# Kernel optimization log

Measured on AMD Instinct MI355X. Metric: run time of the kernel, lower is better.

The kernel has to match this reference:

```python
import jax, jax.numpy as jnp
import numpy as np

B = 8          # batch size (clouds)
NC = 2048      # coarse points per cloud (pos / x)
NF = 8192      # fine points per cloud (pos_skip / x_skip)
C = 256        # coarse feature dim
CS = 64        # skip feature dim
OUT = 256      # MLP output dim
K = 3          # knn_interpolate k (FPParams default)
EPS = 1e-16    # PyG clamp epsilon on squared distance


def setup_inputs() -> dict:
    key = jax.random.key(0)
    ks = jax.random.split(key, 8)
    x = jax.random.normal(ks[0], (B * NC, C), dtype=jnp.float32)
    pos = jax.random.normal(ks[1], (B * NC, 3), dtype=jnp.float32)
    x_skip = jax.random.normal(ks[2], (B * NF, CS), dtype=jnp.float32)
    pos_skip = jax.random.normal(ks[3], (B * NF, 3), dtype=jnp.float32)
    # contiguous, sorted batch assignments (standard PyG layout)
    batch = jnp.repeat(jnp.arange(B, dtype=jnp.int64), NC)
    batch_skip = jnp.repeat(jnp.arange(B, dtype=jnp.int64), NF)
    W1 = jax.random.normal(ks[4], (C + CS, OUT), dtype=jnp.float32) * (1.0 / np.sqrt(C + CS))
    b1 = jnp.zeros((OUT,), dtype=jnp.float32)
    W2 = jax.random.normal(ks[5], (OUT, OUT), dtype=jnp.float32) * (1.0 / np.sqrt(OUT))
    b2 = jnp.zeros((OUT,), dtype=jnp.float32)
    return {"x": x, "pos": pos, "batch": batch, "x_skip": x_skip,
            "pos_skip": pos_skip, "batch_skip": batch_skip,
            "W1": W1, "b1": b1, "W2": W2, "b2": b2}


def _knn_interpolate(x, pos, pos_skip):
    # x: [B*NC, C], pos: [B*NC, 3], pos_skip: [B*NF, 3]
    posb = pos.reshape(B, NC, 3)
    posf = pos_skip.reshape(B, NF, 3)
    xb = x.reshape(B, NC, -1)
    # squared pairwise distances per cloud: [B, NF, NC]
    d2 = jnp.sum((posf[:, :, None, :] - posb[:, None, :, :]) ** 2, axis=-1)
    neg_d2, idx = jax.lax.top_k(-d2, K)          # k nearest -> [B, NF, K]
    d2k = -neg_d2
    w = 1.0 / jnp.maximum(d2k, EPS)              # inverse squared-distance weights
    w = w / jnp.sum(w, axis=-1, keepdims=True)   # [B, NF, K]
    gathered = jax.vmap(lambda xv, iv: xv[iv])(xb, idx)  # [B, NF, K, C]
    out = jnp.sum(gathered * w[..., None], axis=2)       # [B, NF, C]
    return out.reshape(B * NF, -1)


def reference(x, pos, batch, x_skip, pos_skip, batch_skip, W1, b1, W2, b2):
    # 1) interpolate coarse features onto fine points (pos.shape[0] != pos_skip.shape[0])
    xi = _knn_interpolate(x, pos, pos_skip)        # [B*NF, C]
    # 2) concat skip features
    h = jnp.concatenate([xi, x_skip], axis=1)      # [B*NF, C+CS]
    # 3) MLP: Linear -> ReLU -> Linear -> ReLU
    h = jax.nn.relu(h @ W1 + b1)
    h = jax.nn.relu(h @ W2 + b2)
    return (h, pos_skip, batch_skip)
```

## Files before the change

### kernel.cpp

```cpp
#include <hip/hip_runtime.h>
#include <hip/hip_bf16.h>

#define BATCH 8
#define NC 2048
#define NF 8192
#define CDIM 256
#define CSKIP 64
#define OUTD 256
#define MTOT (BATCH*NF)
#define NCTOT (BATCH*NC)
#define NCHUNK 8
#define CHSZ (NC/NCHUNK)

typedef __attribute__((ext_vector_type(8))) short short8;
typedef __attribute__((ext_vector_type(4))) float floatx4;

static __device__ __forceinline__ ushort f2bf(float f) {
    union { float f; unsigned u; } v; v.f = f;
    unsigned r = v.u + 0x7fffu + ((v.u >> 16) & 1u);
    return (ushort)(r >> 16);
}
static __device__ __forceinline__ float bf2f(ushort u) {
    union { unsigned u; float f; } v; v.u = ((unsigned)u) << 16;
    return v.f;
}

#if defined(__has_builtin) && __has_builtin(__builtin_amdgcn_fmed3f)
#define MED3F(a, b, c) __builtin_amdgcn_fmed3f((a), (b), (c))
#else
static __device__ __forceinline__ float MED3F(float a, float b, float c) {
    return fmaxf(fminf(a, b), fminf(fmaxf(a, b), c));
}
#endif

#define TOP3_INS(d, jj, D0, D1, D2, I0, I1, I2)     \
    {                                               \
        bool c2 = (d) < D2, c1 = (d) < D1, c0 = (d) < D0; \
        I2 = c1 ? I1 : (c2 ? (jj) : I2);            \
        I1 = c0 ? I0 : (c1 ? (jj) : I1);            \
        I0 = c0 ? (jj) : I0;                        \
        D2 = MED3F(D1, D2, (d));                    \
        D1 = MED3F(D0, D1, (d));                    \
        D0 = fminf(D0, (d));                        \
    }

#define SEG0 1048576
#define SEG1 1048576
#define SEG5 16384
#define SEG6 (MTOT*3)
#define SEG7 MTOT
#define PREP_THREADS (SEG0+SEG1+SEG5+SEG6+SEG7)

__global__ __launch_bounds__(256) void prep_kernel(const float* __restrict__ x,
                                                   const float* __restrict__ x_skip,
                                                   const float* __restrict__ pos,
                                                   const float* __restrict__ pos_skip,
                                                   ushort* __restrict__ xb,
                                                   ushort* __restrict__ xsb,
                                                   float4* __restrict__ pos4,
                                                   float* __restrict__ out) {
    int t = blockIdx.x * 256 + threadIdx.x;
    if (t < SEG0) {
        float4 v = ((const float4*)x)[t];
        ushort4 p; p.x = f2bf(v.x); p.y = f2bf(v.y); p.z = f2bf(v.z); p.w = f2bf(v.w);
        ((ushort4*)xb)[t] = p;
        return;
    }
    t -= SEG0;
    if (t < SEG1) {
        float4 v = ((const float4*)x_skip)[t];
        ushort4 p; p.x = f2bf(v.x); p.y = f2bf(v.y); p.z = f2bf(v.z); p.w = f2bf(v.w);
        ((ushort4*)xsb)[t] = p;
        return;
    }
    t -= SEG1;
    if (t < SEG5) {
        float4 q;
        q.x = pos[t * 3 + 0]; q.y = pos[t * 3 + 1]; q.z = pos[t * 3 + 2]; q.w = 0.f;
        pos4[t] = q;
        return;
    }
    t -= SEG5;
    if (t < SEG6) {
        out[(size_t)MTOT * OUTD + t] = pos_skip[t];
        return;
    }
    t -= SEG6;
    if (t < SEG7) {
        out[(size_t)MTOT * OUTD + (size_t)MTOT * 3 + t] = (float)(t >> 13);
    }
}

__global__ __launch_bounds__(256) void prep_w(const float* __restrict__ W1,
                                              const float* __restrict__ W2,
                                              ushort* __restrict__ Bt1a,
                                              ushort* __restrict__ Bt1b,
                                              ushort* __restrict__ Bt2) {
    __shared__ ushort tile[64 * 65];
    int bid = blockIdx.x;
    const float* src; ushort* dst; int k0, n0, KD;
    if (bid < 16)      { src = W1;             dst = Bt1a; k0 = (bid >> 2) * 64; n0 = (bid & 3) * 64; KD = 256; }
    else if (bid < 20) { src = W1 + 256 * 256; dst = Bt1b; k0 = 0;               n0 = (bid - 16) * 64; KD = 64; }
    else               { int b2 = bid - 20; src = W2; dst = Bt2; k0 = (b2 >> 2) * 64; n0 = (b2 & 3) * 64; KD = 256; }
    int tx = threadIdx.x & 63, ty = threadIdx.x >> 6;
#pragma unroll
    for (int r = 0; r < 64; r += 4) {
        int k = r + ty;
        tile[k * 65 + tx] = f2bf(src[(size_t)(k0 + k) * 256 + n0 + tx]);
    }
    __syncthreads();
#pragma unroll
    for (int r = 0; r < 64; r += 4) {
        int n = r + ty;
        dst[(size_t)(n0 + n) * KD + k0 + tx] = tile[tx * 65 + n];
    }
}

__global__ __launch_bounds__(256) void knn_part(const float4* __restrict__ pos4,
                                                const float* __restrict__ pos_skip,
                                                int* __restrict__ pidx,
                                                float* __restrict__ pdst) {
    __shared__ float sx[CHSZ], sy[CHSZ], sz[CHSZ];
    int c = blockIdx.x & (NCHUNK - 1);
    int mA = (blockIdx.x >> 3) * 512 + threadIdx.x;
    int mB = mA + 256;
    int b = mA >> 13;
    int jbase = b * NC + c * CHSZ;

    float4 q0 = pos4[jbase + threadIdx.x];
    sx[threadIdx.x] = q0.x; sy[threadIdx.x] = q0.y; sz[threadIdx.x] = q0.z;
    float pxA = pos_skip[mA * 3 + 0];
    float pyA = pos_skip[mA * 3 + 1];
    float pzA = pos_skip[mA * 3 + 2];
    float pxB = pos_skip[mB * 3 + 0];
    float pyB = pos_skip[mB * 3 + 1];
    float pzB = pos_skip[mB * 3 + 2];
    __syncthreads();

    float dA0 = 1e30f, dA1 = 1e30f, dA2 = 1e30f;
    float dB0 = 1e30f, dB1 = 1e30f, dB2 = 1e30f;
    int iA0 = jbase, iA1 = jbase, iA2 = jbase;
    int iB0 = jbase, iB1 = jbase, iB2 = jbase;
#pragma unroll 2
    for (int j4 = 0; j4 < CHSZ; j4 += 4) {
        float4 qx = *(const float4*)&sx[j4];
        float4 qy = *(const float4*)&sy[j4];
        float4 qz = *(const float4*)&sz[j4];
#pragma unroll
        for (int u = 0; u < 4; ++u) {
            int jj = jbase + j4 + u;
            float ax = pxA - qx[u], ay = pyA - qy[u], az = pzA - qz[u];
            float dA = ax * ax + ay * ay + az * az;
            TOP3_INS(dA, jj, dA0, dA1, dA2, iA0, iA1, iA2);
            float bx = pxB - qx[u], by = pyB - qy[u], bz = pzB - qz[u];
            float dB = bx * bx + by * by + bz * bz;
            TOP3_INS(dB, jj, dB0, dB1, dB2, iB0, iB1, iB2);
        }
    }
    size_t baseA = ((size_t)c * MTOT + mA) * 3;
    pdst[baseA + 0] = dA0; pdst[baseA + 1] = dA1; pdst[baseA + 2] = dA2;
    pidx[baseA + 0] = iA0; pidx[baseA + 1] = iA1; pidx[baseA + 2] = iA2;
    size_t baseB = ((size_t)c * MTOT + mB) * 3;
    pdst[baseB + 0] = dB0; pdst[baseB + 1] = dB1; pdst[baseB + 2] = dB2;
    pidx[baseB + 0] = iB0; pidx[baseB + 1] = iB1; pidx[baseB + 2] = iB2;
}

__global__ __launch_bounds__(64) void knn_merge(const int* __restrict__ pidx,
                                                const float* __restrict__ pdst,
                                                int* __restrict__ idxw,
                                                float* __restrict__ wgt) {
    int m = blockIdx.x * 64 + threadIdx.x;
    float d0 = 1e30f, d1 = 1e30f, d2 = 1e30f;
    int i0 = 0, i1 = 0, i2 = 0;
#pragma unroll
    for (int c = 0; c < NCHUNK; ++c) {
        size_t base = ((size_t)c * MTOT + m) * 3;
#pragma unroll
        for (int s = 0; s < 3; ++s) {
            float d = pdst[base + s];
            int jj = pidx[base + s];
            TOP3_INS(d, jj, d0, d1, d2, i0, i1, i2);
        }
    }
    float w0 = 1.0f / fmaxf(d0, 1e-16f);
    float w1 = 1.0f / fmaxf(d1, 1e-16f);
    float w2 = 1.0f / fmaxf(d2, 1e-16f);
    float inv = 1.0f / (w0 + w1 + w2);
    idxw[m * 3 + 0] = i0;  wgt[m * 3 + 0] = w0 * inv;
    idxw[m * 3 + 1] = i1;  wgt[m * 3 + 1] = w1 * inv;
    idxw[m * 3 + 2] = i2;  wgt[m * 3 + 2] = w2 * inv;
}

#define GW_STRIDE 72
__global__ __launch_bounds__(256) void gemm_G(const ushort* __restrict__ A,
                                              const ushort* __restrict__ Bt,
                                              ushort* __restrict__ Gb) {
    __shared__ ushort wB[256 * GW_STRIDE];
    int tid = threadIdx.x;
    int wave = tid >> 6, lane = tid & 63;
    int m0 = blockIdx.x * 64 + wave * 16;
    int lrow = lane & 15;
    int ko = (lane >> 4) * 8;

    floatx4 acc[16];
#pragma unroll
    for (int i = 0; i < 16; ++i) acc[i] = (floatx4){0.f, 0.f, 0.f, 0.f};

    for (int s = 0; s < 4; ++s) {
        if (s) __syncthreads();
        for (int cch = tid; cch < 2048; cch += 256) {
            int n = cch >> 3, koff = (cch & 7) * 8;
            *(short8*)&wB[n * GW_STRIDE + koff] = *(const short8*)(Bt + n * 256 + s * 64 + koff);
        }
        __syncthreads();
        const ushort* ar = A + (size_t)(m0 + lrow) * 256 + s * 64 + ko;
#pragma unroll
        for (int k0 = 0; k0 < 64; k0 += 32) {
            short8 af = *(const short8*)(ar + k0);
#pragma unroll
            for (int nt = 0; nt < 16; ++nt) {
                short8 bf = *(const short8*)&wB[(nt * 16 + lrow) * GW_STRIDE + k0 + ko];
                acc[nt] = __builtin_amdgcn_mfma_f32_16x16x32_bf16(af, bf, acc[nt], 0, 0, 0);
            }
        }
    }
    int rbase = (lane >> 4) * 4;
#pragma unroll
    for (int nt = 0; nt < 16; ++nt) {
        int n = nt * 16 + lrow;
#pragma unroll
        for (int r = 0; r < 4; ++r)
            Gb[(size_t)(m0 + rbase + r) * 256 + n] = f2bf(acc[nt][r]);
    }
}

#define LDS_STRIDE 264
#define WB_STRIDE 72
__global__ __launch_bounds__(256) void fused_kernel(const ushort* __restrict__ xsb,
                                                    const ushort* __restrict__ Bt1b,
                                                    const ushort* __restrict__ Gb,
                                                    const int* __restrict__ idxw,
                                                    const float* __restrict__ wgt,
                                                    const float* __restrict__ b1,
                                                    const ushort* __restrict__ Bt2,
                                                    const float* __restrict__ b2,
                                                    float* __restrict__ out) {
    __shared__ ushort h1t[4][16 * LDS_STRIDE];
    __shared__ ushort wB[256 * WB_STRIDE];
    __shared__ int   sIdx[4][48];
    __shared__ float sWgt[4][48];
    int tid = threadIdx.x;
    int wave = tid >> 6, lane = tid & 63;
    int m0 = blockIdx.x * 64 + wave * 16;
    int lrow = lane & 15;
    int ko = (lane >> 4) * 8;
    int rbase = (lane >> 4) * 4;

    if (lane < 48) {
        sIdx[wave][lane] = idxw[m0 * 3 + lane];
        sWgt[wave][lane] = wgt[m0 * 3 + lane];
    }

    const ushort4* Gv = (const ushort4*)Gb;
    const int*   si = sIdx[wave];
    const float* sw = sWgt[wave];
    ushort4 g[4][3];
#define GATHER(slot, i) {                                         \
        int a0 = si[(i) * 3 + 0];                                 \
        int a1 = si[(i) * 3 + 1];                                 \
        int a2 = si[(i) * 3 + 2];                                 \
        g[slot][0] = Gv[(size_t)a0 * 64 + lane];                  \
        g[slot][1] = Gv[(size_t)a1 * 64 + lane];                  \
        g[slot][2] = Gv[(size_t)a2 * 64 + lane]; }

    GATHER(0, 0) GATHER(1, 1) GATHER(2, 2) GATHER(3, 3)

    for (int cch = tid; cch < 2048; cch += 256) {
        int n = cch >> 3, koff = (cch & 7) * 8;
        *(short8*)&wB[n * WB_STRIDE + koff] = *(const short8*)(Bt1b + n * 64 + koff);
    }
    __syncthreads();

    floatx4 acc[16];
#pragma unroll
    for (int i = 0; i < 16; ++i) acc[i] = (floatx4){0.f, 0.f, 0.f, 0.f};
    {
        const ushort* arow = xsb + (size_t)(m0 + lrow) * 64 + ko;
#pragma unroll
        for (int k0 = 0; k0 < 64; k0 += 32) {
            short8 af = *(const short8*)(arow + k0);
#pragma unroll
            for (int nt = 0; nt < 16; ++nt) {
                short8 bf = *(const short8*)&wB[(nt * 16 + lrow) * WB_STRIDE + k0 + ko];
                acc[nt] = __builtin_amdgcn_mfma_f32_16x16x32_bf16(af, bf, acc[nt], 0, 0, 0);
            }
        }
    }

    ushort* ht = h1t[wave];
#pragma unroll
    for (int nt = 0; nt < 16; ++nt) {
        int n = nt * 16 + lrow;
#pragma unroll
        for (int r = 0; r < 4; ++r)
            ht[(rbase + r) * LDS_STRIDE + n] = f2bf(acc[nt][r]);
    }

    {
        float4 bv = ((const float4*)b1)[lane];
#define COMBINE(i) {                                              \
        int s = (i) & 3;                                          \
        float w0 = sw[(i) * 3 + 0], w1 = sw[(i) * 3 + 1], w2 = sw[(i) * 3 + 2]; \
        ushort4 sv = *(const ushort4*)(ht + (i) * LDS_STRIDE + 4 * lane); \
        float4 h;                                                 \
        h.x = fmaxf(bf2f(sv.x) + w0 * bf2f(g[s][0].x) + w1 * bf2f(g[s][1].x) + w2 * bf2f(g[s][2].x) + bv.x, 0.f); \
        h.y = fmaxf(bf2f(sv.y) + w0 * bf2f(g[s][0].y) + w1 * bf2f(g[s][1].y) + w2 * bf2f(g[s][2].y) + bv.y, 0.f); \
        h.z = fmaxf(bf2f(sv.z) + w0 * bf2f(g[s][0].z) + w1 * bf2f(g[s][1].z) + w2 * bf2f(g[s][2].z) + bv.z, 0.f); \
        h.w = fmaxf(bf2f(sv.w) + w0 * bf2f(g[s][0].w) + w1 * bf2f(g[s][1].w) + w2 * bf2f(g[s][2].w) + bv.w, 0.f); \
        ushort4 hp;                                               \
        hp.x = f2bf(h.x); hp.y = f2bf(h.y); hp.z = f2bf(h.z); hp.w = f2bf(h.w); \
        *(ushort4*)(ht + (i) * LDS_STRIDE + 4 * lane) = hp; }

#pragma unroll
        for (int i = 0; i < 12; ++i) { COMBINE(i); GATHER(i & 3, i + 4); }
#pragma unroll
        for (int i = 12; i < 16; ++i) { COMBINE(i); }
#undef GATHER
#undef COMBINE
    }

#pragma unroll
    for (int i = 0; i < 16; ++i) acc[i] = (floatx4){0.f, 0.f, 0.f, 0.f};
    for (int s = 0; s < 4; ++s) {
        __syncthreads();
        for (int cch = tid; cch < 2048; cch += 256) {
            int n = cch >> 3, koff = (cch & 7) * 8;
            *(short8*)&wB[n * WB_STRIDE + koff] = *(const short8*)(Bt2 + n * 256 + s * 64 + koff);
        }
        __syncthreads();
        const ushort* ar = ht + lrow * LDS_STRIDE + s * 64 + ko;
#pragma unroll
        for (int k0 = 0; k0 < 64; k0 += 32) {
            short8 af = *(const short8*)(ar + k0);
#pragma unroll
            for (int nt = 0; nt < 16; ++nt) {
                short8 bf = *(const short8*)&wB[(nt * 16 + lrow) * WB_STRIDE + k0 + ko];
                acc[nt] = __builtin_amdgcn_mfma_f32_16x16x32_bf16(af, bf, acc[nt], 0, 0, 0);
            }
        }
    }
#pragma unroll
    for (int nt = 0; nt < 16; ++nt) {
        int n = nt * 16 + lrow;
        float bv2 = b2[n];
#pragma unroll
        for (int r = 0; r < 4; ++r) {
            float v = fmaxf(acc[nt][r] + bv2, 0.f);
            out[(size_t)(m0 + rbase + r) * OUTD + n] = v;
        }
    }
}

extern "C" void kernel_launch(void* const* d_in, const int* in_sizes, int n_in,
                              void* d_out, int out_size, void* d_ws, size_t ws_size,
                              hipStream_t stream) {
    const float* x        = (const float*)d_in[0];
    const float* pos      = (const float*)d_in[1];
    const float* x_skip   = (const float*)d_in[3];
    const float* pos_skip = (const float*)d_in[4];
    const float* W1       = (const float*)d_in[6];
    const float* b1       = (const float*)d_in[7];
    const float* W2       = (const float*)d_in[8];
    const float* b2       = (const float*)d_in[9];

    char* ws = (char*)d_ws;
    size_t off = 0;
    int*    idxw = (int*)(ws + off);    off += (size_t)MTOT * 3 * 4;
    float*  wgt  = (float*)(ws + off);  off += (size_t)MTOT * 3 * 4;
    ushort* xb   = (ushort*)(ws + off); off += (size_t)NCTOT * 256 * 2;
    ushort* xsb  = (ushort*)(ws + off); off += (size_t)MTOT * 64 * 2;
    ushort* Gb   = (ushort*)(ws + off); off += (size_t)NCTOT * 256 * 2;
    ushort* Bt1a = (ushort*)(ws + off); off += (size_t)256 * 256 * 2;
    ushort* Bt1b = (ushort*)(ws + off); off += (size_t)256 * 64 * 2;
    ushort* Bt2  = (ushort*)(ws + off); off += (size_t)256 * 256 * 2;
    float4* pos4 = (float4*)(ws + off); off += (size_t)(NCTOT + 4) * 16;
    float* out = (float*)d_out;
    int*   pidx = (int*)d_out;
    float* pdst = (float*)((char*)d_out + (size_t)NCHUNK * MTOT * 3 * 4);

    prep_kernel<<<(PREP_THREADS + 255) / 256, 256, 0, stream>>>(
        x, x_skip, pos, pos_skip, xb, xsb, pos4, out);
    prep_w<<<36, 256, 0, stream>>>(W1, W2, Bt1a, Bt1b, Bt2);
    knn_part<<<(MTOT / 512) * NCHUNK, 256, 0, stream>>>(pos4, pos_skip, pidx, pdst);
    knn_merge<<<MTOT / 64, 64, 0, stream>>>(pidx, pdst, idxw, wgt);
    gemm_G<<<NCTOT / 64, 256, 0, stream>>>(xb, Bt1a, Gb);
    fused_kernel<<<MTOT / 64, 256, 0, stream>>>(xsb, Bt1b, Gb, idxw, wgt, b1, Bt2, b2, out);
}
```

Measured before the change: 224.7 us.

## Replace chunked KNN plus merge with single full-scan kernel using wave-level skip

Merges the two-stage KNN (per-chunk partial top-3 followed by a merge kernel) into one kernel where each thread scans all coarse points of its cloud from shared memory. Candidate insertion is guarded by a wave-wide __any test against the current third-best distance, so most candidates skip the top-3 insertion logic. This removes the partial-result round trip through global memory and one launch, in exchange for fewer blocks (256), one query per thread, and 24KB of shared memory per block, which lowers parallelism and occupancy.

New measurement: 261.3 us. 1.16x slower.

```diff
diff --git a/kernel.cpp b/kernel.cpp
--- a/kernel.cpp
+++ b/kernel.cpp
@@ -9,8 +9,6 @@
 #define OUTD 256
 #define MTOT (BATCH*NF)
 #define NCTOT (BATCH*NC)
-#define NCHUNK 8
-#define CHSZ (NC/NCHUNK)
 
 typedef __attribute__((ext_vector_type(8))) short short8;
 typedef __attribute__((ext_vector_type(4))) float floatx4;
@@ -116,72 +114,49 @@
     }
 }
 
-__global__ __launch_bounds__(256) void knn_part(const float4* __restrict__ pos4,
+__global__ __launch_bounds__(256) void knn_full(const float4* __restrict__ pos4,
                                                 const float* __restrict__ pos_skip,
-                                                int* __restrict__ pidx,
-                                                float* __restrict__ pdst) {
-    __shared__ float sx[CHSZ], sy[CHSZ], sz[CHSZ];
-    int c = blockIdx.x & (NCHUNK - 1);
-    int mA = (blockIdx.x >> 3) * 512 + threadIdx.x;
-    int mB = mA + 256;
-    int b = mA >> 13;
-    int jbase = b * NC + c * CHSZ;
-
-    float4 q0 = pos4[jbase + threadIdx.x];
-    sx[threadIdx.x] = q0.x; sy[threadIdx.x] = q0.y; sz[threadIdx.x] = q0.z;
-    float pxA = pos_skip[mA * 3 + 0];
-    float pyA = pos_skip[mA * 3 + 1];
-    float pzA = pos_skip[mA * 3 + 2];
-    float pxB = pos_skip[mB * 3 + 0];
-    float pyB = pos_skip[mB * 3 + 1];
-    float pzB = pos_skip[mB * 3 + 2];
-    __syncthreads();
-
-    float dA0 = 1e30f, dA1 = 1e30f, dA2 = 1e30f;
-    float dB0 = 1e30f, dB1 = 1e30f, dB2 = 1e30f;
-    int iA0 = jbase, iA1 = jbase, iA2 = jbase;
-    int iB0 = jbase, iB1 = jbase, iB2 = jbase;
-#pragma unroll 2
-    for (int j4 = 0; j4 < CHSZ; j4 += 4) {
-        float4 qx = *(const float4*)&sx[j4];
-        float4 qy = *(const float4*)&sy[j4];
-        float4 qz = *(const float4*)&sz[j4];
-#pragma unroll
-        for (int u = 0; u < 4; ++u) {
-            int jj = jbase + j4 + u;
-            float ax = pxA - qx[u], ay = pyA - qy[u], az = pzA - qz[u];
-            float dA = ax * ax + ay * ay + az * az;
-            TOP3_INS(dA, jj, dA0, dA1, dA2, iA0, iA1, iA2);
-            float bx = pxB - qx[u], by = pyB - qy[u], bz = pzB - qz[u];
-            float dB = bx * bx + by * by + bz * bz;
-            TOP3_INS(dB, jj, dB0, dB1, dB2, iB0, iB1, iB2);
-        }
-    }
-    size_t baseA = ((size_t)c * MTOT + mA) * 3;
-    pdst[baseA + 0] = dA0; pdst[baseA + 1] = dA1; pdst[baseA + 2] = dA2;
-    pidx[baseA + 0] = iA0; pidx[baseA + 1] = iA1; pidx[baseA + 2] = iA2;
-    size_t baseB = ((size_t)c * MTOT + mB) * 3;
-    pdst[baseB + 0] = dB0; pdst[baseB + 1] = dB1; pdst[baseB + 2] = dB2;
-    pidx[baseB + 0] = iB0; pidx[baseB + 1] = iB1; pidx[baseB + 2] = iB2;
-}
-
-__global__ __launch_bounds__(64) void knn_merge(const int* __restrict__ pidx,
-                                                const float* __restrict__ pdst,
                                                 int* __restrict__ idxw,
                                                 float* __restrict__ wgt) {
-    int m = blockIdx.x * 64 + threadIdx.x;
+    __shared__ float sx[NC], sy[NC], sz[NC];
+    int m = blockIdx.x * 256 + threadIdx.x;
+    int b = m >> 13;
+    int jbase = b * NC;
+    for (int i = threadIdx.x; i < NC; i += 256) {
+        float4 q = pos4[jbase + i];
+        sx[i] = q.x; sy[i] = q.y; sz[i] = q.z;
+    }
+    float px = pos_skip[m * 3 + 0];
+    float py = pos_skip[m * 3 + 1];
+    float pz = pos_skip[m * 3 + 2];
+    __syncthreads();
+
     float d0 = 1e30f, d1 = 1e30f, d2 = 1e30f;
-    int i0 = 0, i1 = 0, i2 = 0;
-#pragma unroll
-    for (int c = 0; c < NCHUNK; ++c) {
-        size_t base = ((size_t)c * MTOT + m) * 3;
-#pragma unroll
-        for (int s = 0; s < 3; ++s) {
-            float d = pdst[base + s];
-            int jj = pidx[base + s];
-            TOP3_INS(d, jj, d0, d1, d2, i0, i1, i2);
-        }
-    }
+    int i0 = jbase, i1 = jbase, i2 = jbase;
+    for (int j8 = 0; j8 < NC; j8 += 8) {
+        float4 qx0 = *(const float4*)&sx[j8];
+        float4 qx1 = *(const float4*)&sx[j8 + 4];
+        float4 qy0 = *(const float4*)&sy[j8];
+        float4 qy1 = *(const float4*)&sy[j8 + 4];
+        float4 qz0 = *(const float4*)&sz[j8];
+        float4 qz1 = *(const float4*)&sz[j8 + 4];
+        float dd[8];
+#pragma unroll
+        for (int u = 0; u < 4; ++u) {
+            float ax = px - qx0[u], ay = py - qy0[u], az = pz - qz0[u];
+            dd[u] = ax * ax + ay * ay + az * az;
+            float bx = px - qx1[u], by = py - qy1[u], bz = pz - qz1[u];
+            dd[u + 4] = bx * bx + by * by + bz * bz;
+        }
+#pragma unroll
+        for (int u = 0; u < 8; ++u) {
+            if (__any(dd[u] < d2)) {
+                int jj = jbase + j8 + u;
+                TOP3_INS(dd[u], jj, d0, d1, d2, i0, i1, i2);
+            }
+        }
+    }
+
     float w0 = 1.0f / fmaxf(d0, 1e-16f);
     float w1 = 1.0f / fmaxf(d1, 1e-16f);
     float w2 = 1.0f / fmaxf(d2, 1e-16f);
@@ -385,14 +360,11 @@
     ushort* Bt2  = (ushort*)(ws + off); off += (size_t)256 * 256 * 2;
     float4* pos4 = (float4*)(ws + off); off += (size_t)(NCTOT + 4) * 16;
     float* out = (float*)d_out;
-    int*   pidx = (int*)d_out;
-    float* pdst = (float*)((char*)d_out + (size_t)NCHUNK * MTOT * 3 * 4);
 
     prep_kernel<<<(PREP_THREADS + 255) / 256, 256, 0, stream>>>(
         x, x_skip, pos, pos_skip, xb, xsb, pos4, out);
     prep_w<<<36, 256, 0, stream>>>(W1, W2, Bt1a, Bt1b, Bt2);
-    knn_part<<<(MTOT / 512) * NCHUNK, 256, 0, stream>>>(pos4, pos_skip, pidx, pdst);
-    knn_merge<<<MTOT / 64, 64, 0, stream>>>(pidx, pdst, idxw, wgt);
+    knn_full<<<MTOT / 256, 256, 0, stream>>>(pos4, pos_skip, idxw, wgt);
     gemm_G<<<NCTOT / 64, 256, 0, stream>>>(xb, Bt1a, Gb);
     fused_kernel<<<MTOT / 64, 256, 0, stream>>>(xsb, Bt1b, Gb, idxw, wgt, b1, Bt2, b2, out);
 }
```
